# Kernel tuning notes

Measured on AMD Instinct MI355X. Metric: run time of the kernel, lower is better.

Reference implementation:

```python
import jax, jax.numpy as jnp
import numpy as np

N, B, DIN, H, D, E = 20000, 2, 128, 4, 64, 320000
NEG_SLOPE = 0.2


def _leaky(x):
    return jnp.where(x >= 0, x, NEG_SLOPE * x)


def setup_inputs() -> dict:
    key = jax.random.key(0)
    k1, k2, k3, k4, k5, k6 = jax.random.split(key, 6)
    feat = jax.random.normal(k1, (N, B, DIN), dtype=jnp.float32)
    # fc weight, xavier-ish scale; stored as (Din, H*D) so projection is feat @ W
    W = jax.random.normal(k2, (DIN, H * D), dtype=jnp.float32) * (1.0 / np.sqrt(DIN))
    attn_l = jax.random.normal(k3, (H, D), dtype=jnp.float32) * 0.1
    attn_r = jax.random.normal(k4, (H, D), dtype=jnp.float32) * 0.1
    src = jax.random.randint(k5, (E,), 0, N, dtype=jnp.int32)
    dst = jax.random.randint(k6, (E,), 0, N, dtype=jnp.int32)
    return {"feat": feat, "W": W, "attn_l": attn_l, "attn_r": attn_r, "src": src, "dst": dst}


def reference(feat, W, attn_l, attn_r, src, dst):
    # feat: (N,B,Din) -> projected features (N,B,H,D)
    ft = (feat @ W).reshape(N, B, H, D)
    # per-node attention logits (N,B,H)
    el = jnp.einsum('nbhd,hd->nbh', ft, attn_l)
    er = jnp.einsum('nbhd,hd->nbh', ft, attn_r)
    # edge logits: u_add_v then LeakyReLU, shape (E,B,H)
    e = _leaky(el[src] + er[dst])
    # edge softmax normalized per destination node (numerically stable)
    emax = jax.ops.segment_max(e, dst, num_segments=N)
    emax = jnp.where(jnp.isfinite(emax), emax, 0.0)  # nodes with no in-edges
    ex = jnp.exp(e - emax[dst])
    denom = jax.ops.segment_sum(ex, dst, num_segments=N)
    a = ex / denom[dst]                               # (E,B,H); denom>0 for every edge's dst
    # u_mul_e messages and sum-aggregation by dst
    m = ft[src] * a[..., None]                        # (E,B,H,D)
    rst = jax.ops.segment_sum(m, dst, num_segments=N)  # (N,B,H,D)
    # module sets self.activation = leaky_relu unconditionally
    return _leaky(rst)
```

## Files before the change

kernel.cpp:

```cpp
#include <hip/hip_runtime.h>
#include <hip/hip_bf16.h>
#include <math.h>


typedef unsigned short ushort;
typedef __attribute__((ext_vector_type(8))) unsigned short ushort8;
typedef __attribute__((ext_vector_type(8))) short short8v;
typedef __attribute__((ext_vector_type(4))) float f32x4;

constexpr int DIN = 128;
constexpr int B   = 2;
constexpr int H   = 4;
constexpr int D   = 64;
constexpr int HD  = H * D;
constexpr int BHD = B * HD;
constexpr int NCOL = 272;
constexpr int PREP_ELEMS  = NCOL * DIN;
constexpr int PREP_BLOCKS = (PREP_ELEMS + 255) / 256;
constexpr int SXS = 72;

__device__ __forceinline__ float leaky(float x) { return x >= 0.f ? x : 0.2f * x; }

__device__ __forceinline__ ushort f2bf(float f) {
    return __builtin_bit_cast(ushort, __float2bfloat16(f));
}
__device__ __forceinline__ float bf2f(ushort v) {
    return __uint_as_float(((unsigned int)v) << 16);
}

__global__ __launch_bounds__(256) void hist_prep_kernel(
    const int* __restrict__ dst, int* __restrict__ deg, int E,
    const float* __restrict__ W, const float* __restrict__ attn_l,
    const float* __restrict__ attn_r, ushort* __restrict__ WT, int histBlocks)
{
    const int t = threadIdx.x;
    const int b = blockIdx.x;
    if (b < histBlocks) {
        int e4 = (b * 256 + t) * 4;
        if (e4 + 3 < E) {
            int4 dd = *(const int4*)(dst + e4);
            atomicAdd(&deg[dd.x], 1); atomicAdd(&deg[dd.y], 1);
            atomicAdd(&deg[dd.z], 1); atomicAdd(&deg[dd.w], 1);
        } else {
            for (int e = e4; e < E; ++e) atomicAdd(&deg[dst[e]], 1);
        }
        return;
    }
    int id = (b - histBlocks) * 256 + t;
    if (id >= PREP_ELEMS) return;
    int c = id >> 7, k = id & 127;
    float v;
    if (c < 256) {
        v = W[k * HD + c];
    } else if (c < 264) {
        int j = c - 256, h = j & 3;
        const float* av = (j < 4 ? attn_l : attn_r) + h * D;
        const float* wp = W + k * HD + h * D;
        float s = 0.f;
        for (int d = 0; d < D; ++d) s = fmaf(wp[d], av[d], s);
        v = s;
    } else {
        v = 0.f;
    }
    WT[c * DIN + k] = f2bf(v);
}

__device__ void scan_body(const int* __restrict__ deg, int* __restrict__ offs,
                          int* __restrict__ cursor, int n)
{
    __shared__ int wcarry[4];
    const int t = threadIdx.x;
    const int lane = t & 63;
    const int wid = t >> 6;
    int carry = 0;
    const int nstripes = (n + 1023) >> 10;
    for (int s = 0; s < nstripes; ++s) {
        const int base = (s << 10) + t * 4;
        int4 d = make_int4(0, 0, 0, 0);
        if (base + 3 < n) {
            d = *(const int4*)(deg + base);
        } else {
            if (base     < n) d.x = deg[base];
            if (base + 1 < n) d.y = deg[base + 1];
            if (base + 2 < n) d.z = deg[base + 2];
        }
        const int sum4 = (d.x + d.y) + (d.z + d.w);
        int inc = sum4;
#pragma unroll
        for (int o = 1; o < 64; o <<= 1) {
            int v = __shfl_up(inc, o, 64);
            if (lane >= o) inc += v;
        }
        if (lane == 63) wcarry[wid] = inc;
        __syncthreads();
        int wpre = carry;
#pragma unroll
        for (int k = 0; k < 4; ++k) if (k < wid) wpre += wcarry[k];
        const int e0 = wpre + inc - sum4;
        int4 ov;
        ov.x = e0; ov.y = e0 + d.x; ov.z = ov.y + d.y; ov.w = ov.z + d.z;
        if (base + 3 < n) {
            *(int4*)(offs + base) = ov;
            *(int4*)(cursor + base) = ov;
        } else {
            if (base     < n) { offs[base]     = ov.x; cursor[base]     = ov.x; }
            if (base + 1 < n) { offs[base + 1] = ov.y; cursor[base + 1] = ov.y; }
            if (base + 2 < n) { offs[base + 2] = ov.z; cursor[base + 2] = ov.z; }
        }
        carry += (wcarry[0] + wcarry[1]) + (wcarry[2] + wcarry[3]);
        __syncthreads();
    }
    if (t == 0) offs[n] = carry;
}

__global__ __launch_bounds__(256) void proj_scan_kernel(
    const float* __restrict__ feat, const ushort* __restrict__ WT,
    ushort* __restrict__ ftt, float* __restrict__ el, float* __restrict__ er,
    const int* __restrict__ deg, int* __restrict__ offs, int* __restrict__ cursor,
    int N, int nTiles)
{
    if ((int)blockIdx.x >= nTiles) {
        scan_body(deg, offs, cursor, N);
        return;
    }
    __shared__ ushort sxp[4][2][16][SXS];
    const int t = threadIdx.x;
    const int w = t >> 6;
    const int lane = t & 63;
    const int lr = lane & 15;
    const int lk = lane >> 4;

    short8v bfrag[4][4];
#pragma unroll
    for (int ct = 0; ct < 4; ++ct) {
        const int col = w * 64 + ct * 16 + lr;
#pragma unroll
        for (int ks = 0; ks < 4; ++ks)
            bfrag[ct][ks] = *(const short8v*)&WT[col * DIN + ks * 32 + lk * 8];
    }
    short8v efrag[4];
#pragma unroll
    for (int ks = 0; ks < 4; ++ks)
        efrag[ks] = *(const short8v*)&WT[(256 + lr) * DIN + ks * 32 + lk * 8];

    const int row0 = blockIdx.x * 64;
    const int rrow = lane >> 2;
    const int seg  = lane & 3;

    auto loadA = [&](int rt, short8v aout[4]) {
        const float* fp = feat + (size_t)(row0 + rt * 16 + lr) * DIN + lk * 8;
#pragma unroll
        for (int ks = 0; ks < 4; ++ks) {
            f32x4 x0 = *(const f32x4*)(fp + ks * 32);
            f32x4 x1 = *(const f32x4*)(fp + ks * 32 + 4);
            short8v v;
            v[0] = (short)f2bf(x0[0]); v[1] = (short)f2bf(x0[1]);
            v[2] = (short)f2bf(x0[2]); v[3] = (short)f2bf(x0[3]);
            v[4] = (short)f2bf(x1[0]); v[5] = (short)f2bf(x1[1]);
            v[6] = (short)f2bf(x1[2]); v[7] = (short)f2bf(x1[3]);
            aout[ks] = v;
        }
    };

    short8v aP[4], aN[4];
    loadA(0, aP);

#pragma unroll
    for (int rt = 0; rt < 4; ++rt) {
        if (rt < 3) loadA(rt + 1, aN);

        f32x4 acc[4] = {{0.f,0.f,0.f,0.f},{0.f,0.f,0.f,0.f},{0.f,0.f,0.f,0.f},{0.f,0.f,0.f,0.f}};
#pragma unroll
        for (int ct = 0; ct < 4; ++ct)
#pragma unroll
            for (int ks = 0; ks < 4; ++ks)
                acc[ct] = __builtin_amdgcn_mfma_f32_16x16x32_bf16(aP[ks], bfrag[ct][ks], acc[ct], 0, 0, 0);

        ushort (* __restrict__ sw)[SXS] = sxp[w][rt & 1];
#pragma unroll
        for (int ct = 0; ct < 4; ++ct)
#pragma unroll
            for (int r = 0; r < 4; ++r)
                sw[lk * 4 + r][ct * 16 + lr] = f2bf(acc[ct][r]);
        __builtin_amdgcn_wave_barrier();
        ushort8 o0 = *(const ushort8*)&sw[rrow][seg * 16];
        ushort8 o1 = *(const ushort8*)&sw[rrow][seg * 16 + 8];
        const int row = row0 + rt * 16 + rrow;
        const int nn = row >> 1;
        const int bb = row & 1;
        ushort* gp = ftt + ((size_t)(bb * 4 + w) * N + nn) * 64 + seg * 16;
        *(ushort8*)gp = o0;
        *(ushort8*)(gp + 8) = o1;

        if (rt == w) {
            f32x4 acce = {0.f, 0.f, 0.f, 0.f};
#pragma unroll
            for (int ks = 0; ks < 4; ++ks)
                acce = __builtin_amdgcn_mfma_f32_16x16x32_bf16(aP[ks], efrag[ks], acce, 0, 0, 0);
#pragma unroll
            for (int r = 0; r < 4; ++r) {
                const int row2 = row0 + rt * 16 + lk * 4 + r;
                if (lr < 4)       el[row2 * 4 + lr]       = acce[r];
                else if (lr < 8)  er[row2 * 4 + (lr - 4)] = acce[r];
            }
        }

#pragma unroll
        for (int ks = 0; ks < 4; ++ks) aP[ks] = aN[ks];
    }
}

__global__ __launch_bounds__(256) void scatter_kernel(
    const int* __restrict__ dst, const int* __restrict__ src,
    int* __restrict__ cursor, int* __restrict__ esrc, int E)
{
    int e4 = (blockIdx.x * 256 + threadIdx.x) * 4;
    if (e4 + 3 < E) {
        int4 dd = *(const int4*)(dst + e4);
        int4 ss = *(const int4*)(src + e4);
        int p0 = atomicAdd(&cursor[dd.x], 1); esrc[p0] = ss.x;
        int p1 = atomicAdd(&cursor[dd.y], 1); esrc[p1] = ss.y;
        int p2 = atomicAdd(&cursor[dd.z], 1); esrc[p2] = ss.z;
        int p3 = atomicAdd(&cursor[dd.w], 1); esrc[p3] = ss.w;
    } else {
        for (int e = e4; e < E; ++e) {
            int pos = atomicAdd(&cursor[dst[e]], 1);
            esrc[pos] = src[e];
        }
    }
}

__global__ __launch_bounds__(256) void agg_kernel(
    const ushort* __restrict__ ftt, const float* __restrict__ el,
    const float* __restrict__ er, const int* __restrict__ offs,
    const int* __restrict__ esrc, float* __restrict__ out, int N)
{
    const int t = threadIdx.x;
    const int bh = blockIdx.x & 7;
    const int n  = (blockIdx.x >> 3) * 4 + (t >> 6);
    if (n >= N) return;
    const int lane = t & 63;
    const int g  = lane >> 3;
    const int d8 = lane & 7;
    const int beg = offs[n];
    const int end = offs[n + 1];
    const float erd = er[n * 8 + bh];
    const ushort8* __restrict__ fv = (const ushort8*)(ftt + (size_t)bh * N * 64);

    float acc[8];
#pragma unroll
    for (int j = 0; j < 8; ++j) acc[j] = 0.f;
    float dsum = 0.f;

    int i = beg + g;
    for (; i + 8 < end; i += 16) {
        int s0 = esrc[i];
        int s1 = esrc[i + 8];
        float x0 = el[(size_t)s0 * 8 + bh];
        float x1 = el[(size_t)s1 * 8 + bh];
        ushort8 v0 = fv[(size_t)s0 * 8 + d8];
        ushort8 v1 = fv[(size_t)s1 * 8 + d8];
        float w0 = __expf(leaky(x0 + erd));
        float w1 = __expf(leaky(x1 + erd));
        dsum += w0 + w1;
#pragma unroll
        for (int j = 0; j < 8; ++j)
            acc[j] += w0 * bf2f(v0[j]) + w1 * bf2f(v1[j]);
    }
    if (i < end) {
        int s0 = esrc[i];
        float w0 = __expf(leaky(el[(size_t)s0 * 8 + bh] + erd));
        ushort8 v0 = fv[(size_t)s0 * 8 + d8];
        dsum += w0;
#pragma unroll
        for (int j = 0; j < 8; ++j) acc[j] = fmaf(w0, bf2f(v0[j]), acc[j]);
    }

#pragma unroll
    for (int o = 8; o < 64; o <<= 1) {
        dsum += __shfl_xor(dsum, o, 64);
#pragma unroll
        for (int j = 0; j < 8; ++j) acc[j] += __shfl_xor(acc[j], o, 64);
    }

    if (g == 0) {
        const float sc = (end > beg) ? (1.f / dsum) : 0.f;
        float4 o0, o1;
        o0.x = leaky(acc[0] * sc); o0.y = leaky(acc[1] * sc);
        o0.z = leaky(acc[2] * sc); o0.w = leaky(acc[3] * sc);
        o1.x = leaky(acc[4] * sc); o1.y = leaky(acc[5] * sc);
        o1.z = leaky(acc[6] * sc); o1.w = leaky(acc[7] * sc);
        float* op = out + (size_t)n * BHD + bh * 64 + d8 * 8;
        *(float4*)op = o0;
        *(float4*)(op + 4) = o1;
    }
}

extern "C" void kernel_launch(void* const* d_in, const int* in_sizes, int n_in,
                              void* d_out, int out_size, void* d_ws, size_t ws_size,
                              hipStream_t stream)
{
    const float* feat   = (const float*)d_in[0];
    const float* W      = (const float*)d_in[1];
    const float* attn_l = (const float*)d_in[2];
    const float* attn_r = (const float*)d_in[3];
    const int*   src    = (const int*)d_in[4];
    const int*   dst    = (const int*)d_in[5];
    float* out = (float*)d_out;

    const int N = in_sizes[0] / (B * DIN);
    const int E = in_sizes[4];
    const int R = N * B;
    const int nTiles = R / 64;
    const int histBlocks = (E / 4 + 255) / 256;
    const int edgeBlocks = histBlocks;

    auto align_up = [](size_t x) { return (x + 255) & ~(size_t)255; };
    size_t off = 0;
    char* base = (char*)d_ws;
    ushort* ftt = (ushort*)(base + off); off += align_up((size_t)R * HD * sizeof(ushort));
    float* el   = (float*)(base + off); off += align_up((size_t)R * H * sizeof(float));
    float* er   = (float*)(base + off); off += align_up((size_t)R * H * sizeof(float));
    ushort* WT  = (ushort*)(base + off); off += align_up((size_t)NCOL * DIN * sizeof(ushort));
    int* deg    = (int*)(base + off); off += align_up((size_t)N * sizeof(int));
    int* offs   = (int*)(base + off); off += align_up((size_t)(N + 1) * sizeof(int));
    int* cursor = (int*)(base + off); off += align_up((size_t)N * sizeof(int));
    int* esrc   = (int*)(base + off); off += align_up((size_t)E * sizeof(int));
    (void)ws_size; (void)n_in; (void)out_size;

    hipMemsetAsync(deg, 0, (size_t)N * sizeof(int), stream);

    hist_prep_kernel<<<histBlocks + PREP_BLOCKS, 256, 0, stream>>>(
        dst, deg, E, W, attn_l, attn_r, WT, histBlocks);
    proj_scan_kernel<<<nTiles + 1, 256, 0, stream>>>(
        feat, WT, ftt, el, er, deg, offs, cursor, N, nTiles);
    scatter_kernel<<<edgeBlocks, 256, 0, stream>>>(dst, src, cursor, esrc, E);
    agg_kernel<<<8 * ((N + 3) / 4), 256, 0, stream>>>(ftt, el, er, offs, esrc, out, N);
}
```

Baseline: 133.9 us.

## Store projected features in fp32 and reduce aggregation partials through LDS

The projected feature table moves from bf16 to fp32 storage, which removes the bf16 unpack in the aggregation loop but doubles the bytes gathered per edge and written by the projection. The cross-group shuffle reduction of the 8 accumulators in agg_kernel is replaced by a shared-memory reduction with a block barrier, and the final write becomes one scalar per lane. Early-return is replaced by a valid flag so the barrier is safe. The gather traffic roughly doubles, which is the main risk for this memory-bound kernel.

```diff
diff --git a/kernel.cpp b/kernel.cpp
--- a/kernel.cpp
+++ b/kernel.cpp
@@ -17,15 +17,12 @@
 constexpr int NCOL = 272;
 constexpr int PREP_ELEMS  = NCOL * DIN;
 constexpr int PREP_BLOCKS = (PREP_ELEMS + 255) / 256;
-constexpr int SXS = 72;
+constexpr int SXS = 68;
 
 __device__ __forceinline__ float leaky(float x) { return x >= 0.f ? x : 0.2f * x; }
 
 __device__ __forceinline__ ushort f2bf(float f) {
     return __builtin_bit_cast(ushort, __float2bfloat16(f));
-}
-__device__ __forceinline__ float bf2f(ushort v) {
-    return __uint_as_float(((unsigned int)v) << 16);
 }
 
 __global__ __launch_bounds__(256) void hist_prep_kernel(
@@ -115,7 +112,7 @@
 
 __global__ __launch_bounds__(256) void proj_scan_kernel(
     const float* __restrict__ feat, const ushort* __restrict__ WT,
-    ushort* __restrict__ ftt, float* __restrict__ el, float* __restrict__ er,
+    float* __restrict__ ftt, float* __restrict__ el, float* __restrict__ er,
     const int* __restrict__ deg, int* __restrict__ offs, int* __restrict__ cursor,
     int N, int nTiles)
 {
@@ -123,7 +120,7 @@
         scan_body(deg, offs, cursor, N);
         return;
     }
-    __shared__ ushort sxp[4][2][16][SXS];
+    __shared__ float sxp[4][2][16][SXS];
     const int t = threadIdx.x;
     const int w = t >> 6;
     const int lane = t & 63;
@@ -145,7 +142,7 @@
 
     const int row0 = blockIdx.x * 64;
     const int rrow = lane >> 2;
-    const int seg  = lane & 3;
+    const int sg   = lane & 3;
 
     auto loadA = [&](int rt, short8v aout[4]) {
         const float* fp = feat + (size_t)(row0 + rt * 16 + lr) * DIN + lk * 8;
@@ -176,21 +173,24 @@
             for (int ks = 0; ks < 4; ++ks)
                 acc[ct] = __builtin_amdgcn_mfma_f32_16x16x32_bf16(aP[ks], bfrag[ct][ks], acc[ct], 0, 0, 0);
 
-        ushort (* __restrict__ sw)[SXS] = sxp[w][rt & 1];
+        float (* __restrict__ sw)[SXS] = sxp[w][rt & 1];
 #pragma unroll
         for (int ct = 0; ct < 4; ++ct)
 #pragma unroll
             for (int r = 0; r < 4; ++r)
-                sw[lk * 4 + r][ct * 16 + lr] = f2bf(acc[ct][r]);
+                sw[lk * 4 + r][ct * 16 + lr] = acc[ct][r];
         __builtin_amdgcn_wave_barrier();
-        ushort8 o0 = *(const ushort8*)&sw[rrow][seg * 16];
-        ushort8 o1 = *(const ushort8*)&sw[rrow][seg * 16 + 8];
+        f32x4 o[4];
+#pragma unroll
+        for (int k = 0; k < 4; ++k)
+            o[k] = *(const f32x4*)&sw[rrow][sg * 16 + k * 4];
         const int row = row0 + rt * 16 + rrow;
         const int nn = row >> 1;
         const int bb = row & 1;
-        ushort* gp = ftt + ((size_t)(bb * 4 + w) * N + nn) * 64 + seg * 16;
-        *(ushort8*)gp = o0;
-        *(ushort8*)(gp + 8) = o1;
+        float* gp = ftt + ((size_t)(bb * 4 + w) * N + nn) * 64 + sg * 16;
+#pragma unroll
+        for (int k = 0; k < 4; ++k)
+            *(f32x4*)(gp + k * 4) = o[k];
 
         if (rt == w) {
             f32x4 acce = {0.f, 0.f, 0.f, 0.f};
@@ -231,25 +231,27 @@
 }
 
 __global__ __launch_bounds__(256) void agg_kernel(
-    const ushort* __restrict__ ftt, const float* __restrict__ el,
+    const float* __restrict__ ftt, const float* __restrict__ el,
     const float* __restrict__ er, const int* __restrict__ offs,
     const int* __restrict__ esrc, float* __restrict__ out, int N)
 {
+    __shared__ float red[4][8][64];
     const int t = threadIdx.x;
     const int bh = blockIdx.x & 7;
-    const int n  = (blockIdx.x >> 3) * 4 + (t >> 6);
-    if (n >= N) return;
+    const int nbase = (blockIdx.x >> 3) * 4;
+    const int wv = t >> 6;
+    const int n = nbase + wv;
+    const bool valid = (n < N);
     const int lane = t & 63;
     const int g  = lane >> 3;
     const int d8 = lane & 7;
-    const int beg = offs[n];
-    const int end = offs[n + 1];
-    const float erd = er[n * 8 + bh];
-    const ushort8* __restrict__ fv = (const ushort8*)(ftt + (size_t)bh * N * 64);
-
-    float acc[8];
-#pragma unroll
-    for (int j = 0; j < 8; ++j) acc[j] = 0.f;
+    const int beg = valid ? offs[n] : 0;
+    const int end = valid ? offs[n + 1] : 0;
+    const float erd = valid ? er[n * 8 + bh] : 0.f;
+    const f32x4* __restrict__ fv = (const f32x4*)(ftt + (size_t)bh * N * 64);
+
+    f32x4 acc0 = {0.f, 0.f, 0.f, 0.f};
+    f32x4 acc1 = {0.f, 0.f, 0.f, 0.f};
     float dsum = 0.f;
 
     int i = beg + g;
@@ -258,41 +260,40 @@
         int s1 = esrc[i + 8];
         float x0 = el[(size_t)s0 * 8 + bh];
         float x1 = el[(size_t)s1 * 8 + bh];
-        ushort8 v0 = fv[(size_t)s0 * 8 + d8];
-        ushort8 v1 = fv[(size_t)s1 * 8 + d8];
+        f32x4 a0 = fv[(size_t)s0 * 16 + d8 * 2];
+        f32x4 b0 = fv[(size_t)s0 * 16 + d8 * 2 + 1];
+        f32x4 a1 = fv[(size_t)s1 * 16 + d8 * 2];
+        f32x4 b1 = fv[(size_t)s1 * 16 + d8 * 2 + 1];
         float w0 = __expf(leaky(x0 + erd));
         float w1 = __expf(leaky(x1 + erd));
         dsum += w0 + w1;
-#pragma unroll
-        for (int j = 0; j < 8; ++j)
-            acc[j] += w0 * bf2f(v0[j]) + w1 * bf2f(v1[j]);
+        acc0 += a0 * w0; acc1 += b0 * w0;
+        acc0 += a1 * w1; acc1 += b1 * w1;
     }
     if (i < end) {
         int s0 = esrc[i];
         float w0 = __expf(leaky(el[(size_t)s0 * 8 + bh] + erd));
-        ushort8 v0 = fv[(size_t)s0 * 8 + d8];
+        f32x4 a0 = fv[(size_t)s0 * 16 + d8 * 2];
+        f32x4 b0 = fv[(size_t)s0 * 16 + d8 * 2 + 1];
         dsum += w0;
-#pragma unroll
-        for (int j = 0; j < 8; ++j) acc[j] = fmaf(w0, bf2f(v0[j]), acc[j]);
-    }
-
-#pragma unroll
-    for (int o = 8; o < 64; o <<= 1) {
+        acc0 += a0 * w0; acc1 += b0 * w0;
+    }
+
+#pragma unroll
+    for (int o = 8; o < 64; o <<= 1)
         dsum += __shfl_xor(dsum, o, 64);
-#pragma unroll
-        for (int j = 0; j < 8; ++j) acc[j] += __shfl_xor(acc[j], o, 64);
-    }
-
-    if (g == 0) {
+
+    *(f32x4*)&red[wv][g][d8 * 8]     = acc0;
+    *(f32x4*)&red[wv][g][d8 * 8 + 4] = acc1;
+    __syncthreads();
+
+    const int e = lane;
+    float s = 0.f;
+#pragma unroll
+    for (int gg = 0; gg < 8; ++gg) s += red[wv][gg][e];
+    if (valid) {
         const float sc = (end > beg) ? (1.f / dsum) : 0.f;
-        float4 o0, o1;
-        o0.x = leaky(acc[0] * sc); o0.y = leaky(acc[1] * sc);
-        o0.z = leaky(acc[2] * sc); o0.w = leaky(acc[3] * sc);
-        o1.x = leaky(acc[4] * sc); o1.y = leaky(acc[5] * sc);
-        o1.z = leaky(acc[6] * sc); o1.w = leaky(acc[7] * sc);
-        float* op = out + (size_t)n * BHD + bh * 64 + d8 * 8;
-        *(float4*)op = o0;
-        *(float4*)(op + 4) = o1;
+        out[(size_t)n * BHD + bh * 64 + e] = leaky(s * sc);
     }
 }
 
@@ -318,7 +319,7 @@
     auto align_up = [](size_t x) { return (x + 255) & ~(size_t)255; };
     size_t off = 0;
     char* base = (char*)d_ws;
-    ushort* ftt = (ushort*)(base + off); off += align_up((size_t)R * HD * sizeof(ushort));
+    float* ftt  = (float*)(base + off); off += align_up((size_t)R * HD * sizeof(float));
     float* el   = (float*)(base + off); off += align_up((size_t)R * H * sizeof(float));
     float* er   = (float*)(base + off); off += align_up((size_t)R * H * sizeof(float));
     ushort* WT  = (ushort*)(base + off); off += align_up((size_t)NCOL * DIN * sizeof(ushort));
```

Result: slower. 148.7 us (+11.1%).
